# Performance work log

Measured on AMD Instinct MI355X. Metric: run time of the kernel, lower is better.

## Reference

```python
import jax, jax.numpy as jnp
import numpy as np

HEADS = 16
DIM_HEAD = 64


def setup_inputs() -> dict:
    key = jax.random.key(0)
    k1, k2, k3 = jax.random.split(key, 3)
    b, n, dim = 8, 4096, 1024
    inner = HEADS * DIM_HEAD  # 1024
    x = jax.random.normal(k1, (b, n, dim), dtype=jnp.float32)
    # torch Linear stored transposed; here W_qkv is [in, out] so y = x @ W_qkv
    W_qkv = jax.random.normal(k2, (dim, 4 * inner), dtype=jnp.float32) * (dim ** -0.5)
    W_out = jax.random.normal(k3, (inner, dim), dtype=jnp.float32) * (inner ** -0.5)
    b_out = jnp.zeros((dim,), dtype=jnp.float32)
    return {"x": x, "W_qkv": W_qkv, "W_out": W_out, "b_out": b_out}


def reference(x, W_qkv, W_out, b_out):
    b, n, dim = x.shape
    h, d = HEADS, DIM_HEAD
    scale = d ** -0.5
    qkv = x @ W_qkv  # [b, n, 4*h*d]
    q, k, v, v2 = jnp.split(qkv, 4, axis=-1)
    # rearrange 'b n (h d) -> b h n d'
    to_heads = lambda t: t.reshape(b, n, h, d).transpose(0, 2, 1, 3)
    q, k, v, v2 = map(to_heads, (q, k, v, v2))
    # channel-wise attention: dots = q^T @ k over the sequence axis -> [b,h,d,d]
    dots = jnp.einsum('bhnd,bhne->bhde', q, k) * scale
    attn = jax.nn.softmax(dots, axis=-1)
    # v^T @ v2 -> [b,h,d,d]
    vv = jnp.einsum('bhnd,bhne->bhde', v, v2)
    out = jnp.einsum('bhde,bhef->bhdf', attn, vv)  # [b,h,d,d]
    # rearrange 'b h n d -> b n (h d)' with n == dim_head here
    out = out.transpose(0, 2, 1, 3).reshape(b, d, h * d)  # [b, dim_head, inner]
    return out @ W_out + b_out  # [b, dim_head, dim]
```

## Files before the change

### kernel.cpp

```cpp
#include <hip/hip_runtime.h>
#include <hip/hip_bf16.h>
#include <stdint.h>

typedef _Float16 f16;
typedef _Float16 f16x8 __attribute__((ext_vector_type(8)));
typedef float f32x4 __attribute__((ext_vector_type(4)));

#define AS1 __attribute__((address_space(1)))
#define AS3 __attribute__((address_space(3)))

__global__ __launch_bounds__(256) void tr_cvt_kernel(
    const float* __restrict__ src, f16* __restrict__ dst, int R, int C)
{
    __shared__ float tile[64][65];
    const int b = blockIdx.z;
    src += (size_t)b * R * C;
    dst += (size_t)b * R * C;
    const int c0 = blockIdx.x * 64;
    const int r0 = blockIdx.y * 64;
    const int t = threadIdx.x;
    {
        const int cc = (t & 15) * 4;
        const int rr = t >> 4;
#pragma unroll
        for (int p = 0; p < 4; ++p) {
            const int r = rr + p * 16;
            const float4 v = *(const float4*)(src + (size_t)(r0 + r) * C + c0 + cc);
            tile[r][cc + 0] = v.x; tile[r][cc + 1] = v.y;
            tile[r][cc + 2] = v.z; tile[r][cc + 3] = v.w;
        }
    }
    __syncthreads();
    {
        const int rq = (t & 15) * 4;
        const int cp = t >> 4;
#pragma unroll
        for (int p = 0; p < 4; ++p) {
            const int c = cp + p * 16;
            ushort4 o;
            f16 h0 = (f16)tile[rq + 0][c];
            f16 h1 = (f16)tile[rq + 1][c];
            f16 h2 = (f16)tile[rq + 2][c];
            f16 h3 = (f16)tile[rq + 3][c];
            o.x = __builtin_bit_cast(unsigned short, h0);
            o.y = __builtin_bit_cast(unsigned short, h1);
            o.z = __builtin_bit_cast(unsigned short, h2);
            o.w = __builtin_bit_cast(unsigned short, h3);
            *(ushort4*)(dst + (size_t)(c0 + c) * R + r0 + rq) = o;
        }
    }
}

__device__ __forceinline__ void stage256(
    const f16* __restrict__ src, int ld, char* ldsbase, int tid)
{
    const int lane = tid & 63;
    const int gch = ((lane & 7) ^ (lane >> 3)) * 8;
    const int rowl = tid >> 3;
    const int wbase = (tid >> 3) & ~7;
#pragma unroll
    for (int p = 0; p < 4; ++p) {
        const f16* s = src + (size_t)(p * 64 + rowl) * ld + gch;
        __builtin_amdgcn_global_load_lds(
            (const AS1 uint32_t*)s,
            (AS3 uint32_t*)(ldsbase + (p * 64 + wbase) * 128), 16, 0, 0);
    }
}

__device__ __forceinline__ void gemm256_core(
    const f16* __restrict__ A, const f16* __restrict__ Bt,
    int lda, int ldb, int nsteps,
    f16* As, f16* Bs, f32x4 (&acc)[8][4], int tid)
{
    const int lane = tid & 63, w = tid >> 6;
    const int wr = w >> 2, wc = w & 3;
    const int cl = lane & 15, kg = lane >> 4, b7 = lane & 7;

    stage256(A, lda, (char*)As, tid);
    stage256(Bt, ldb, (char*)Bs, tid);
    asm volatile("s_waitcnt vmcnt(0)" ::: "memory");
    __builtin_amdgcn_s_barrier();

#pragma unroll 1
    for (int t = 0; t < nsteps; ++t) {
        const int cur = t & 1;
        if (t + 1 < nsteps) {
            const int k0 = (t + 1) * 64;
            stage256(A + k0, lda, (char*)As + (cur ^ 1) * 32768, tid);
            stage256(Bt + k0, ldb, (char*)Bs + (cur ^ 1) * 32768, tid);
        }
        const f16* Ab = As + cur * 16384;
        const f16* Bb = Bs + cur * 16384;
#pragma unroll
        for (int kk = 0; kk < 2; ++kk) {
            const int ch = (kk * 4 + kg) ^ b7;
            f16x8 af[8], bf[4];
#pragma unroll
            for (int i = 0; i < 8; ++i)
                af[i] = *(const f16x8*)&Ab[(wr * 128 + i * 16 + cl) * 64 + ch * 8];
#pragma unroll
            for (int j = 0; j < 4; ++j)
                bf[j] = *(const f16x8*)&Bb[(wc * 64 + j * 16 + cl) * 64 + ch * 8];
            __builtin_amdgcn_s_setprio(1);
#pragma unroll
            for (int i = 0; i < 8; ++i)
#pragma unroll
                for (int j = 0; j < 4; ++j)
                    acc[i][j] = __builtin_amdgcn_mfma_f32_16x16x32_f16(af[i], bf[j], acc[i][j], 0, 0, 0);
            __builtin_amdgcn_s_setprio(0);
        }
        asm volatile("s_waitcnt vmcnt(0)" ::: "memory");
        __builtin_amdgcn_s_barrier();
    }
}

__global__ __launch_bounds__(512, 2) void gemm_syk256(
    const f16* __restrict__ xT, f16* __restrict__ Gp)
{
    __shared__ f16 As[2 * 256 * 64];
    __shared__ f16 Bs[2 * 256 * 64];
    const int orig = blockIdx.x;
    const int l = (orig & 7) * 32 + (orig >> 3);
    const int tile = l & 15, b = (l >> 4) & 7, s = l >> 7;
    const int ti = tile >> 2, tj = tile & 3;

    const f16* base = xT + (size_t)b * (1024 * 4096) + (size_t)s * 2048;
    const f16* A  = base + (size_t)ti * 256 * 4096;
    const f16* Bt = base + (size_t)tj * 256 * 4096;

    f32x4 acc[8][4];
#pragma unroll
    for (int i = 0; i < 8; ++i)
#pragma unroll
        for (int j = 0; j < 4; ++j) acc[i][j] = f32x4{0.f, 0.f, 0.f, 0.f};

    gemm256_core(A, Bt, 4096, 4096, 32, As, Bs, acc, threadIdx.x);

    f16* out = Gp + ((size_t)s * 8 + b) * 1048576;
    const int lane = threadIdx.x & 63, w = threadIdx.x >> 6;
    const int wr = w >> 2, wc = w & 3;
    const int cl = lane & 15, rg = lane >> 4;
#pragma unroll
    for (int i = 0; i < 8; ++i)
#pragma unroll
        for (int j = 0; j < 4; ++j)
#pragma unroll
            for (int q = 0; q < 4; ++q) {
                const int row = ti * 256 + wr * 128 + i * 16 + rg * 4 + q;
                const int col = tj * 256 + wc * 64 + j * 16 + cl;
                out[(size_t)row * 1024 + col] = (f16)acc[i][j][q];
            }
}

__global__ __launch_bounds__(256) void reduce_sum(
    const f16* __restrict__ Gp, f16* __restrict__ G)
{
    const size_t i = ((size_t)blockIdx.x * 256 + threadIdx.x) * 8;
    const f16x8 a = *(const f16x8*)(Gp + i);
    const f16x8 c = *(const f16x8*)(Gp + 8388608 + i);
    f16x8 o;
#pragma unroll
    for (int j = 0; j < 8; ++j) o[j] = (f16)((float)a[j] + (float)c[j]);
    *(f16x8*)(G + i) = o;
}

__global__ __launch_bounds__(512, 2) void gemm_qv256(
    const f16* __restrict__ WqkvT, const f16* __restrict__ G,
    f16* __restrict__ UW2)
{
    __shared__ f16 As[2 * 256 * 64];
    __shared__ f16 Bs[2 * 256 * 64];
    const int orig = blockIdx.x;
    const int l = (orig & 7) * 32 + (orig >> 3);
    const int bx = l & 3, by = (l >> 2) & 7, b = l >> 5;
    const int arow = (by < 4) ? by * 256 : 2048 + (by - 4) * 256;

    const f16* A  = WqkvT + (size_t)arow * 1024;
    const f16* Bt = G + (size_t)b * 1048576 + (size_t)bx * 256 * 1024;

    f32x4 acc[8][4];
#pragma unroll
    for (int i = 0; i < 8; ++i)
#pragma unroll
        for (int j = 0; j < 4; ++j) acc[i][j] = f32x4{0.f, 0.f, 0.f, 0.f};

    gemm256_core(A, Bt, 1024, 1024, 16, As, Bs, acc, threadIdx.x);

    f16* C = UW2 + (size_t)b * 2097152;
    const int lane = threadIdx.x & 63, w = threadIdx.x >> 6;
    const int wr = w >> 2, wc = w & 3;
    const int cl = lane & 15, rg = lane >> 4;
#pragma unroll
    for (int i = 0; i < 8; ++i)
#pragma unroll
        for (int j = 0; j < 4; ++j) {
            const int cc = bx * 256 + wc * 64 + j * 16 + cl;
#pragma unroll
            for (int q = 0; q < 4; ++q) {
                const int rr = by * 256 + wr * 128 + i * 16 + rg * 4 + q;
                C[(size_t)rr * 1024 + cc] = (f16)acc[i][j][q];
            }
        }
}

__device__ __forceinline__ void gemm_body(
    const f16* __restrict__ A, const f16* __restrict__ Bt,
    int lda, int ldb, int K, f16* As, f16* Bs,
    f32x4 (&acc)[4][4], int tid)
{
    const int lane = tid & 63, w = tid >> 6;
    const int wr = w >> 1, wc = w & 1;
    const int lrow = lane >> 3;
    const int lcol = (lane & 7) * 8;
    for (int k0 = 0; k0 < K; k0 += 64) {
#pragma unroll
        for (int p = 0; p < 4; ++p) {
            const f16* sa = A + (size_t)(p * 32 + w * 8 + lrow) * lda + k0 + lcol;
            __builtin_amdgcn_global_load_lds(
                (const AS1 uint32_t*)sa,
                (AS3 uint32_t*)((char*)As + p * 4096 + w * 1024), 16, 0, 0);
            const f16* sb = Bt + (size_t)(p * 32 + w * 8 + lrow) * ldb + k0 + lcol;
            __builtin_amdgcn_global_load_lds(
                (const AS1 uint32_t*)sb,
                (AS3 uint32_t*)((char*)Bs + p * 4096 + w * 1024), 16, 0, 0);
        }
        __syncthreads();
#pragma unroll
        for (int kk = 0; kk < 2; ++kk) {
            f16x8 af[4], bfr[4];
#pragma unroll
            for (int i = 0; i < 4; ++i)
                af[i] = *(const f16x8*)&As[(wr * 64 + i * 16 + (lane & 15)) * 64 + kk * 32 + (lane >> 4) * 8];
#pragma unroll
            for (int j = 0; j < 4; ++j)
                bfr[j] = *(const f16x8*)&Bs[(wc * 64 + j * 16 + (lane & 15)) * 64 + kk * 32 + (lane >> 4) * 8];
#pragma unroll
            for (int i = 0; i < 4; ++i)
#pragma unroll
                for (int j = 0; j < 4; ++j)
                    acc[i][j] = __builtin_amdgcn_mfma_f32_16x16x32_f16(af[i], bfr[j], acc[i][j], 0, 0, 0);
        }
        __syncthreads();
    }
}

__global__ __launch_bounds__(256) void gemm_out(
    const f16* __restrict__ A, const f16* __restrict__ Bt,
    const float* __restrict__ bias, float* __restrict__ Cout)
{
    __shared__ f16 As[128 * 64];
    __shared__ f16 Bs[128 * 64];
    const int tn0 = blockIdx.x * 128;
    const int tm0 = blockIdx.y * 128;
    f32x4 acc[4][4];
#pragma unroll
    for (int i = 0; i < 4; ++i)
#pragma unroll
        for (int j = 0; j < 4; ++j) acc[i][j] = f32x4{0.f, 0.f, 0.f, 0.f};

    gemm_body(A + (size_t)tm0 * 1024, Bt + (size_t)tn0 * 1024,
              1024, 1024, 1024, As, Bs, acc, threadIdx.x);

    const int lane = threadIdx.x & 63, w = threadIdx.x >> 6;
    const int wr = w >> 1, wc = w & 1;
    const int cl = lane & 15, rg = lane >> 4;
#pragma unroll
    for (int i = 0; i < 4; ++i)
#pragma unroll
        for (int j = 0; j < 4; ++j) {
            const int cc = tn0 + wc * 64 + j * 16 + cl;
            const float bv = bias[cc];
#pragma unroll
            for (int q = 0; q < 4; ++q) {
                const int rr = tm0 + wr * 64 + i * 16 + rg * 4 + q;
                Cout[(size_t)rr * 1024 + cc] = acc[i][j][q] + bv;
            }
        }
}

__global__ __launch_bounds__(512) void attn_small(
    const f16* __restrict__ UW2, const f16* __restrict__ WqkvT,
    f16* __restrict__ O)
{
    __shared__ float dots[64][66];
    __shared__ float vv[64][66];
    const int h = blockIdx.x, b = blockIdx.y;
    const int tid = threadIdx.x, lane = tid & 63, w = tid >> 6;
    const int isVV = w >> 2;
    const int kq = w & 3;

    const f16* Arows = UW2 + (size_t)b * (2048 * 1024)
                           + (size_t)isVV * (1024 * 1024) + (size_t)h * 64 * 1024;
    const f16* Brows = WqkvT + (size_t)(isVV ? 3072 : 1024) * 1024 + (size_t)h * 64 * 1024;

    f32x4 acc[4][4];
#pragma unroll
    for (int i = 0; i < 4; ++i)
#pragma unroll
        for (int j = 0; j < 4; ++j) acc[i][j] = f32x4{0.f, 0.f, 0.f, 0.f};

    const int cl = lane & 15, kg = lane >> 4;
    for (int ks = 0; ks < 8; ++ks) {
        const int k0 = kq * 256 + ks * 32 + kg * 8;
        f16x8 af[4], bfr[4];
#pragma unroll
        for (int i = 0; i < 4; ++i)
            af[i] = *(const f16x8*)(Arows + (size_t)(i * 16 + cl) * 1024 + k0);
#pragma unroll
        for (int j = 0; j < 4; ++j)
            bfr[j] = *(const f16x8*)(Brows + (size_t)(j * 16 + cl) * 1024 + k0);
#pragma unroll
        for (int i = 0; i < 4; ++i)
#pragma unroll
            for (int j = 0; j < 4; ++j)
                acc[i][j] = __builtin_amdgcn_mfma_f32_16x16x32_f16(af[i], bfr[j], acc[i][j], 0, 0, 0);
    }

    float (*dst)[66] = isVV ? vv : dots;
#pragma unroll
    for (int r = 0; r < 4; ++r) {
        if (kq == r) {
            if (r == 0) {
#pragma unroll
                for (int i = 0; i < 4; ++i)
#pragma unroll
                    for (int j = 0; j < 4; ++j)
#pragma unroll
                        for (int q = 0; q < 4; ++q)
                            dst[i * 16 + kg * 4 + q][j * 16 + cl] = acc[i][j][q];
            } else {
#pragma unroll
                for (int i = 0; i < 4; ++i)
#pragma unroll
                    for (int j = 0; j < 4; ++j)
#pragma unroll
                        for (int q = 0; q < 4; ++q)
                            dst[i * 16 + kg * 4 + q][j * 16 + cl] += acc[i][j][q];
            }
        }
        __syncthreads();
    }

    if (tid < 64) {
        const int r = tid;
        float mx = -1e30f;
        for (int e = 0; e < 64; ++e) {
            const float v = dots[r][e] * 0.125f;
            dots[r][e] = v;
            mx = fmaxf(mx, v);
        }
        float s = 0.f;
        for (int e = 0; e < 64; ++e) {
            const float v = __expf(dots[r][e] - mx);
            dots[r][e] = v;
            s += v;
        }
        const float inv = 1.f / s;
        for (int e = 0; e < 64; ++e) dots[r][e] *= inv;
    }
    __syncthreads();

    {
        const int r = tid >> 3, f0 = (tid & 7) * 8;
        float o[8];
#pragma unroll
        for (int i = 0; i < 8; ++i) o[i] = 0.f;
        for (int e = 0; e < 64; ++e) {
            const float a = dots[r][e];
#pragma unroll
            for (int i = 0; i < 8; ++i) o[i] += a * vv[e][f0 + i];
        }
        f16* Od = O + (size_t)b * 64 * 1024 + (size_t)r * 1024 + h * 64 + f0;
#pragma unroll
        for (int i = 0; i < 8; ++i) Od[i] = (f16)o[i];
    }
}

extern "C" void kernel_launch(void* const* d_in, const int* in_sizes, int n_in,
                              void* d_out, int out_size, void* d_ws, size_t ws_size,
                              hipStream_t stream)
{
    const float* x    = (const float*)d_in[0];
    const float* Wqkv = (const float*)d_in[1];
    const float* Wout = (const float*)d_in[2];
    const float* bout = (const float*)d_in[3];

    char* ws = (char*)d_ws;
    f16* xT    = (f16*)(ws + 0);
    f16* WqkvT = (f16*)(ws + 67108864);
    f16* WoutT = (f16*)(ws + 75497472);
    f16* G     = (f16*)(ws + 77594624);
    f16* Gp    = (f16*)(ws + 94371840);
    f16* UW2   = (f16*)(ws + 94371840);
    f16* O     = (f16*)(ws + 127926272);

    tr_cvt_kernel<<<dim3(16, 64, 8), 256, 0, stream>>>(x, xT, 4096, 1024);
    tr_cvt_kernel<<<dim3(64, 16, 1), 256, 0, stream>>>(Wqkv, WqkvT, 1024, 4096);
    tr_cvt_kernel<<<dim3(16, 16, 1), 256, 0, stream>>>(Wout, WoutT, 1024, 1024);

    gemm_syk256<<<256, 512, 0, stream>>>(xT, Gp);
    reduce_sum<<<4096, 256, 0, stream>>>(Gp, G);
    gemm_qv256<<<256, 512, 0, stream>>>(WqkvT, G, UW2);
    attn_small<<<dim3(16, 8), 512, 0, stream>>>(UW2, WqkvT, O);
    gemm_out<<<dim3(8, 4), 256, 0, stream>>>(O, WoutT, bout, (float*)d_out);
}
```

Baseline: 204.2 us.

## Fuse x transpose-convert into Gram GEMM and rework pipeline waits

The Gram GEMM now reads fp32 x directly, converting to fp16 in registers and writing transposed, swizzled tiles into LDS. This removes the separate 128MB-scale transpose/convert kernel and its workspace round trip. The shared gemm256_core also switches to a partial vmcnt wait with a barrier at loop top, and drops the setprio hints. The trade-off is heavier register use and per-thread conversion work inside the GEMM main loop.

```diff
diff --git a/kernel.cpp b/kernel.cpp
--- a/kernel.cpp
+++ b/kernel.cpp
@@ -51,6 +51,136 @@
     }
 }
 
+__device__ __forceinline__ void load_f32(
+    const float* __restrict__ Ag, const float* __restrict__ Bg,
+    int kb, int w, int lane, float4 (&a4)[8], float4 (&b4)[8])
+{
+#pragma unroll
+    for (int p = 0; p < 8; ++p)
+        a4[p] = *(const float4*)(Ag + (size_t)(kb + w * 8 + p) * 1024 + lane * 4);
+#pragma unroll
+    for (int p = 0; p < 8; ++p)
+        b4[p] = *(const float4*)(Bg + (size_t)(kb + w * 8 + p) * 1024 + lane * 4);
+}
+
+__device__ __forceinline__ void write_f16(
+    f16* Aw, f16* Bw, int w, int lane,
+    const float4 (&a4)[8], const float4 (&b4)[8])
+{
+    const int c = w ^ (lane & 7);
+#pragma unroll
+    for (int i = 0; i < 4; ++i) {
+        f16x8 ha, hb;
+#pragma unroll
+        for (int p = 0; p < 8; ++p) {
+            const float4 va = a4[p];
+            const float4 vb = b4[p];
+            ha[p] = (f16)((i == 0) ? va.x : (i == 1) ? va.y : (i == 2) ? va.z : va.w);
+            hb[p] = (f16)((i == 0) ? vb.x : (i == 1) ? vb.y : (i == 2) ? vb.z : vb.w);
+        }
+        *(f16x8*)&Aw[(lane * 4 + i) * 64 + c * 8] = ha;
+        *(f16x8*)&Bw[(lane * 4 + i) * 64 + c * 8] = hb;
+    }
+}
+
+__global__ __launch_bounds__(512, 2) void gemm_syk256(
+    const float* __restrict__ x, f16* __restrict__ Gp)
+{
+    __shared__ f16 As[2 * 256 * 64];
+    __shared__ f16 Bs[2 * 256 * 64];
+    const int orig = blockIdx.x;
+    const int l = (orig & 7) * 32 + (orig >> 3);
+    const int tile = l & 15, b = (l >> 4) & 7, s = l >> 7;
+    const int ti = tile >> 2, tj = tile & 3;
+
+    const float* base = x + (size_t)b * (4096 * 1024) + (size_t)s * 2048 * 1024;
+    const float* Ag = base + ti * 256;
+    const float* Bg = base + tj * 256;
+
+    const int tid = threadIdx.x;
+    const int lane = tid & 63, w = tid >> 6;
+    const int wr = w >> 2, wc = w & 3;
+    const int cl = lane & 15, kg = lane >> 4;
+
+    f32x4 acc[8][4];
+#pragma unroll
+    for (int i = 0; i < 8; ++i)
+#pragma unroll
+        for (int j = 0; j < 4; ++j) acc[i][j] = f32x4{0.f, 0.f, 0.f, 0.f};
+
+    {
+        float4 a4[8], b4[8];
+        load_f32(Ag, Bg, 0, w, lane, a4, b4);
+        write_f16(As, Bs, w, lane, a4, b4);
+        asm volatile("s_waitcnt lgkmcnt(0)" ::: "memory");
+        __builtin_amdgcn_s_barrier();
+    }
+
+#pragma unroll 1
+    for (int t = 0; t < 32; ++t) {
+        const int cur = t & 1;
+        float4 a4[8], b4[8];
+        if (t + 1 < 32)
+            load_f32(Ag, Bg, (t + 1) * 64, w, lane, a4, b4);
+
+        const f16* Ab = As + cur * 16384;
+        const f16* Bb = Bs + cur * 16384;
+#pragma unroll
+        for (int kk = 0; kk < 2; ++kk) {
+            f16x8 af[8], bf[4];
+#pragma unroll
+            for (int i = 0; i < 8; ++i) {
+                const int m = wr * 128 + i * 16 + cl;
+                const int c = (kk * 4 + kg) ^ ((m >> 2) & 7);
+                af[i] = *(const f16x8*)&Ab[m * 64 + c * 8];
+            }
+#pragma unroll
+            for (int j = 0; j < 4; ++j) {
+                const int m = wc * 64 + j * 16 + cl;
+                const int c = (kk * 4 + kg) ^ ((m >> 2) & 7);
+                bf[j] = *(const f16x8*)&Bb[m * 64 + c * 8];
+            }
+            __builtin_amdgcn_s_setprio(1);
+#pragma unroll
+            for (int i = 0; i < 8; ++i)
+#pragma unroll
+                for (int j = 0; j < 4; ++j)
+                    acc[i][j] = __builtin_amdgcn_mfma_f32_16x16x32_f16(af[i], bf[j], acc[i][j], 0, 0, 0);
+            __builtin_amdgcn_s_setprio(0);
+        }
+        if (t + 1 < 32)
+            write_f16(As + (cur ^ 1) * 16384, Bs + (cur ^ 1) * 16384,
+                      w, lane, a4, b4);
+        asm volatile("s_waitcnt lgkmcnt(0)" ::: "memory");
+        __builtin_amdgcn_s_barrier();
+    }
+
+    f16* out = Gp + ((size_t)s * 8 + b) * 1048576;
+    const int rg = lane >> 4;
+#pragma unroll
+    for (int i = 0; i < 8; ++i)
+#pragma unroll
+        for (int j = 0; j < 4; ++j)
+#pragma unroll
+            for (int q = 0; q < 4; ++q) {
+                const int row = ti * 256 + wr * 128 + i * 16 + rg * 4 + q;
+                const int col = tj * 256 + wc * 64 + j * 16 + cl;
+                out[(size_t)row * 1024 + col] = (f16)acc[i][j][q];
+            }
+}
+
+__global__ __launch_bounds__(256) void reduce_sum(
+    const f16* __restrict__ Gp, f16* __restrict__ G)
+{
+    const size_t i = ((size_t)blockIdx.x * 256 + threadIdx.x) * 8;
+    const f16x8 a = *(const f16x8*)(Gp + i);
+    const f16x8 c = *(const f16x8*)(Gp + 8388608 + i);
+    f16x8 o;
+#pragma unroll
+    for (int j = 0; j < 8; ++j) o[j] = (f16)((float)a[j] + (float)c[j]);
+    *(f16x8*)(G + i) = o;
+}
+
 __device__ __forceinline__ void stage256(
     const f16* __restrict__ src, int ld, char* ldsbase, int tid)
 {
@@ -78,8 +208,6 @@
 
     stage256(A, lda, (char*)As, tid);
     stage256(Bt, ldb, (char*)Bs, tid);
-    asm volatile("s_waitcnt vmcnt(0)" ::: "memory");
-    __builtin_amdgcn_s_barrier();
 
 #pragma unroll 1
     for (int t = 0; t < nsteps; ++t) {
@@ -88,7 +216,11 @@
             const int k0 = (t + 1) * 64;
             stage256(A + k0, lda, (char*)As + (cur ^ 1) * 32768, tid);
             stage256(Bt + k0, ldb, (char*)Bs + (cur ^ 1) * 32768, tid);
-        }
+            asm volatile("s_waitcnt vmcnt(8)" ::: "memory");
+        } else {
+            asm volatile("s_waitcnt vmcnt(0)" ::: "memory");
+        }
+        __builtin_amdgcn_s_barrier();
         const f16* Ab = As + cur * 16384;
         const f16* Bb = Bs + cur * 16384;
 #pragma unroll
@@ -101,67 +233,14 @@
 #pragma unroll
             for (int j = 0; j < 4; ++j)
                 bf[j] = *(const f16x8*)&Bb[(wc * 64 + j * 16 + cl) * 64 + ch * 8];
-            __builtin_amdgcn_s_setprio(1);
 #pragma unroll
             for (int i = 0; i < 8; ++i)
 #pragma unroll
                 for (int j = 0; j < 4; ++j)
                     acc[i][j] = __builtin_amdgcn_mfma_f32_16x16x32_f16(af[i], bf[j], acc[i][j], 0, 0, 0);
-            __builtin_amdgcn_s_setprio(0);
-        }
-        asm volatile("s_waitcnt vmcnt(0)" ::: "memory");
+        }
         __builtin_amdgcn_s_barrier();
     }
-}
-
-__global__ __launch_bounds__(512, 2) void gemm_syk256(
-    const f16* __restrict__ xT, f16* __restrict__ Gp)
-{
-    __shared__ f16 As[2 * 256 * 64];
-    __shared__ f16 Bs[2 * 256 * 64];
-    const int orig = blockIdx.x;
-    const int l = (orig & 7) * 32 + (orig >> 3);
-    const int tile = l & 15, b = (l >> 4) & 7, s = l >> 7;
-    const int ti = tile >> 2, tj = tile & 3;
-
-    const f16* base = xT + (size_t)b * (1024 * 4096) + (size_t)s * 2048;
-    const f16* A  = base + (size_t)ti * 256 * 4096;
-    const f16* Bt = base + (size_t)tj * 256 * 4096;
-
-    f32x4 acc[8][4];
-#pragma unroll
-    for (int i = 0; i < 8; ++i)
-#pragma unroll
-        for (int j = 0; j < 4; ++j) acc[i][j] = f32x4{0.f, 0.f, 0.f, 0.f};
-
-    gemm256_core(A, Bt, 4096, 4096, 32, As, Bs, acc, threadIdx.x);
-
-    f16* out = Gp + ((size_t)s * 8 + b) * 1048576;
-    const int lane = threadIdx.x & 63, w = threadIdx.x >> 6;
-    const int wr = w >> 2, wc = w & 3;
-    const int cl = lane & 15, rg = lane >> 4;
-#pragma unroll
-    for (int i = 0; i < 8; ++i)
-#pragma unroll
-        for (int j = 0; j < 4; ++j)
-#pragma unroll
-            for (int q = 0; q < 4; ++q) {
-                const int row = ti * 256 + wr * 128 + i * 16 + rg * 4 + q;
-                const int col = tj * 256 + wc * 64 + j * 16 + cl;
-                out[(size_t)row * 1024 + col] = (f16)acc[i][j][q];
-            }
-}
-
-__global__ __launch_bounds__(256) void reduce_sum(
-    const f16* __restrict__ Gp, f16* __restrict__ G)
-{
-    const size_t i = ((size_t)blockIdx.x * 256 + threadIdx.x) * 8;
-    const f16x8 a = *(const f16x8*)(Gp + i);
-    const f16x8 c = *(const f16x8*)(Gp + 8388608 + i);
-    f16x8 o;
-#pragma unroll
-    for (int j = 0; j < 8; ++j) o[j] = (f16)((float)a[j] + (float)c[j]);
-    *(f16x8*)(G + i) = o;
 }
 
 __global__ __launch_bounds__(512, 2) void gemm_qv256(
@@ -386,19 +465,17 @@
     const float* bout = (const float*)d_in[3];
 
     char* ws = (char*)d_ws;
-    f16* xT    = (f16*)(ws + 0);
-    f16* WqkvT = (f16*)(ws + 67108864);
-    f16* WoutT = (f16*)(ws + 75497472);
-    f16* G     = (f16*)(ws + 77594624);
-    f16* Gp    = (f16*)(ws + 94371840);
-    f16* UW2   = (f16*)(ws + 94371840);
-    f16* O     = (f16*)(ws + 127926272);
-
-    tr_cvt_kernel<<<dim3(16, 64, 8), 256, 0, stream>>>(x, xT, 4096, 1024);
+    f16* WqkvT = (f16*)(ws + 0);
+    f16* WoutT = (f16*)(ws + 8388608);
+    f16* G     = (f16*)(ws + 10485760);
+    f16* Gp    = (f16*)(ws + 27262976);
+    f16* UW2   = (f16*)(ws + 27262976);
+    f16* O     = (f16*)(ws + 60817408);
+
     tr_cvt_kernel<<<dim3(64, 16, 1), 256, 0, stream>>>(Wqkv, WqkvT, 1024, 4096);
     tr_cvt_kernel<<<dim3(16, 16, 1), 256, 0, stream>>>(Wout, WoutT, 1024, 1024);
 
-    gemm_syk256<<<256, 512, 0, stream>>>(xT, Gp);
+    gemm_syk256<<<256, 512, 0, stream>>>(x, Gp);
     reduce_sum<<<4096, 256, 0, stream>>>(Gp, G);
     gemm_qv256<<<256, 512, 0, stream>>>(WqkvT, G, UW2);
     attn_small<<<dim3(16, 8), 512, 0, stream>>>(UW2, WqkvT, O);
```

Result: slower. 238.3 us (+16.7%).
